# Optimization experiments

Hardware: AMD Instinct MI355X
Metric: run time of the kernel (lower is better)

The kernel has to match this reference:

```python
import jax, jax.numpy as jnp
import numpy as np

KH = KW = 3
SH = SW = 1
PH = PW = 1


def _im2col(x, kh, kw, sh, sw, ph, pw):
    # x: [N, C, H, W] -> cols: [N, C*kh*kw, H_out*W_out], ordering (C, kh, kw)
    N, C, H, W = x.shape
    H_out = (H + 2 * ph - kh) // sh + 1
    W_out = (W + 2 * pw - kw) // sw + 1
    x_pad = jnp.pad(x, ((0, 0), (0, 0), (ph, ph), (pw, pw)))
    # fixed small loop over kernel offsets (kh*kw = 9), strided slices
    patches = [x_pad[:, :, i:i + sh * H_out:sh, j:j + sw * W_out:sw]
               for i in range(kh) for j in range(kw)]  # each [N, C, H_out, W_out]
    cols = jnp.stack(patches, axis=2)  # [N, C, kh*kw, H_out, W_out]
    cols = cols.reshape(N, C * kh * kw, H_out * W_out)
    return cols, H_out, W_out


def setup_inputs() -> dict:
    key = jax.random.key(0)
    k1, k2, k3 = jax.random.split(key, 3)
    x = jax.random.normal(k1, (16, 128, 56, 56), dtype=jnp.float32)
    weight = jax.random.normal(k2, (256, 128, 3, 3), dtype=jnp.float32) * 0.05
    fan_in = 128 * 3 * 3
    bound = 1.0 / fan_in ** 0.5
    bias = jax.random.uniform(k3, (256,), dtype=jnp.float32, minval=-bound, maxval=bound)
    return {"x": x, "weight": weight, "bias": bias}


def reference(x, weight, bias):
    # im2col unfold + (analog) matmul conv; noise_cfg=None -> plain matmul
    cols, H_out, W_out = _im2col(x, KH, KW, SH, SW, PH, PW)  # [N, K, L]
    N = cols.shape[0]
    Cout = weight.shape[0]
    Wmat = weight.reshape(Cout, -1)  # [Cout, K], K = C*kh*kw
    # y[n, l, o] = sum_k cols[n, k, l] * Wmat[o, k]  (AnalogMatMulFn without noise)
    y = jnp.einsum('nkl,ok->nol', cols, Wmat)  # [N, Cout, L]
    y = y.reshape(N, Cout, H_out, W_out)
    y = y + bias[None, :, None, None]
    return y
```

## Files before the change

kernel.cpp:

```cpp
#include <hip/hip_runtime.h>
#include <hip/hip_bf16.h>
#include <stdint.h>


typedef __attribute__((ext_vector_type(8))) short short8;
typedef __attribute__((ext_vector_type(4))) float floatx4;

__device__ static inline void gload_lds16(const void* g, void* l) {
  typedef const __attribute__((address_space(1))) unsigned int* gp_t;
  typedef __attribute__((address_space(3))) unsigned int* lp_t;
  __builtin_amdgcn_global_load_lds((gp_t)(uintptr_t)g, (lp_t)(uint32_t)(uintptr_t)l,
                                   16, 0, 0);
}

__global__ __launch_bounds__(256)
void pre_kernel(const float* __restrict__ x, const float* __restrict__ wsrc,
                __hip_bfloat16* __restrict__ xp, __hip_bfloat16* __restrict__ wt) {
  const int b = blockIdx.x;
  if (b < 16 * 58) {
    const int n = b / 58, hp = b % 58;
    __hip_bfloat16* dst = xp + (size_t)(n * 58 + hp) * 58 * 128;
    if (hp == 0 || hp == 57) {
      const uint4 z = {0, 0, 0, 0};
      uint4* p = (uint4*)dst;
      for (int i = threadIdx.x; i < 928; i += 256) p[i] = z;
      return;
    }
    const int h = hp - 1;
    __shared__ float tile[128][57];
    const float* src = x + (size_t)n * (128 * 3136) + h * 56;
    for (int i = threadIdx.x; i < 128 * 14; i += 256) {
      const int c = i / 14, q = i - c * 14;
      const float4 v = ((const float4*)(src + (size_t)c * 3136))[q];
      tile[c][4 * q + 0] = v.x;
      tile[c][4 * q + 1] = v.y;
      tile[c][4 * q + 2] = v.z;
      tile[c][4 * q + 3] = v.w;
    }
    __syncthreads();
    if (threadIdx.x < 32) {
      const uint4 z = {0, 0, 0, 0};
      const int col = (threadIdx.x >> 4) * 57;
      ((uint4*)(dst + (size_t)col * 128))[threadIdx.x & 15] = z;
    }
    __hip_bfloat16* di = dst + 128;
    for (int i = threadIdx.x; i < 56 * 16; i += 256) {
      const int w = i >> 4, c8 = (i & 15) * 8;
      union { uint4 u; __hip_bfloat16 hh[8]; } pk;
#pragma unroll
      for (int j = 0; j < 8; ++j) pk.hh[j] = __float2bfloat16(tile[c8 + j][w]);
      *(uint4*)(di + (size_t)w * 128 + c8) = pk.u;
    }
  } else {
    const int base = (b - 928) * 256 + threadIdx.x;
    for (int t = base; t < 256 * 9 * 128; t += 36 * 256) {
      const int c = t & 127;
      const int kq = (t >> 7) % 9;
      const int cout = t / (9 * 128);
      wt[t] = __float2bfloat16(wsrc[(size_t)(cout * 128 + c) * 9 + kq]);
    }
  }
}

__global__ __launch_bounds__(256)
void conv_gemm_kernel(const __hip_bfloat16* __restrict__ xp,
                      const __hip_bfloat16* __restrict__ wt,
                      const float* __restrict__ bias,
                      float* __restrict__ out) {
  __shared__ __align__(16) __hip_bfloat16 As[128 * 64];
  __shared__ __align__(16) __hip_bfloat16 Bs[128 * 64];

  const int tid = threadIdx.x;
  const int lane = tid & 63;
  const int wave = tid >> 6;
  const int wm = wave >> 1, wn = wave & 1;

  const int id = blockIdx.x;
  const int xcd = id & 7;
  const int r = id >> 3;
  const int mt_ = r / 49;
  const int nt_ = xcd * 49 + (r - mt_ * 49);
  const int m0 = mt_ * 128;
  const int n0 = nt_ * 128;

  const char* wtb = (const char*)wt;
  const char* xpb = (const char*)xp;
  const char* gA[4];
  const char* gB[4];
  char* lA[4];
  char* lB[4];
#pragma unroll
  for (int i = 0; i < 4; ++i) {
    const int f = (i * 256 + tid) * 16;
    const int row = f >> 7;
    const int sub = (f >> 4) & 7;
    const int cb = (sub ^ (row & 7)) << 4;
    gA[i] = wtb + (size_t)(m0 + row) * 2304 + cb;
    const int pix = n0 + row;
    const int nimg = pix / 3136;
    const int rem = pix - nimg * 3136;
    const int hh = rem / 56;
    const int ww = rem - hh * 56;
    gB[i] = xpb + (size_t)((nimg * 58 + hh) * 58 + ww) * 256 + cb;
    lA[i] = (char*)As + i * 4096 + wave * 1024;
    lB[i] = (char*)Bs + i * 4096 + wave * 1024;
  }

  const int quad = lane >> 4;
  const int x7 = lane & 7;
  const int arow = (wm * 64 + (lane & 15)) * 128;
  const int brow = (wn * 64 + (lane & 15)) * 128;
  int cko[2];
  cko[0] = ((0 + quad) ^ x7) << 4;
  cko[1] = ((4 + quad) ^ x7) << 4;

  floatx4 acc[4][4];
#pragma unroll
  for (int a = 0; a < 4; ++a)
#pragma unroll
    for (int c = 0; c < 4; ++c) acc[a][c] = (floatx4)0.f;

#pragma unroll 1
  for (int kq = 0; kq < 9; ++kq) {
    const int kh = kq / 3;
    const int kw_ = kq - kh * 3;
    const int btap = (kh * 58 + kw_) * 256;
#pragma unroll 1
    for (int ch = 0; ch < 2; ++ch) {
      const int aofs = kq * 256 + ch * 128;
      const int bofs = btap + ch * 128;
      __syncthreads();
#pragma unroll
      for (int i = 0; i < 4; ++i) {
        gload_lds16(gA[i] + aofs, lA[i]);
        gload_lds16(gB[i] + bofs, lB[i]);
      }
      __syncthreads();
#pragma unroll
      for (int ks = 0; ks < 2; ++ks) {
        short8 af[4], bf[4];
#pragma unroll
        for (int mt = 0; mt < 4; ++mt)
          af[mt] = *(const short8*)((const char*)As + arow + mt * (16 * 128) + cko[ks]);
#pragma unroll
        for (int nt = 0; nt < 4; ++nt)
          bf[nt] = *(const short8*)((const char*)Bs + brow + nt * (16 * 128) + cko[ks]);
#pragma unroll
        for (int mt = 0; mt < 4; ++mt)
#pragma unroll
          for (int nt = 0; nt < 4; ++nt)
            acc[mt][nt] = __builtin_amdgcn_mfma_f32_16x16x32_bf16(
                af[mt], bf[nt], acc[mt][nt], 0, 0, 0);
      }
    }
  }

  const int col = lane & 15;
  const int rb = (lane >> 4) * 4;
#pragma unroll
  for (int nt = 0; nt < 4; ++nt) {
    const int pix = n0 + wn * 64 + nt * 16 + col;
    const int nimg = pix / 3136;
    const int rem = pix - nimg * 3136;
    float* op = out + (size_t)nimg * (256 * 3136) + rem;
#pragma unroll
    for (int mt = 0; mt < 4; ++mt) {
      const int mb = m0 + wm * 64 + mt * 16 + rb;
#pragma unroll
      for (int rr = 0; rr < 4; ++rr) {
        op[(size_t)(mb + rr) * 3136] = acc[mt][nt][rr] + bias[mb + rr];
      }
    }
  }
}

__global__ __launch_bounds__(256)
void direct_conv_kernel(const float* __restrict__ x, const float* __restrict__ wgt,
                        const float* __restrict__ bias, float* __restrict__ out) {
  const long t = (long)blockIdx.x * 256 + threadIdx.x;
  if (t >= 16L * 256 * 3136) return;
  const int w = t % 56;
  const int h = (t / 56) % 56;
  const int o = (t / 3136) % 256;
  const int n = t / (256L * 3136);
  float s = bias[o];
  for (int c = 0; c < 128; ++c)
    for (int kh = 0; kh < 3; ++kh) {
      const int hh = h + kh - 1;
      if (hh < 0 || hh >= 56) continue;
      for (int kw = 0; kw < 3; ++kw) {
        const int ww = w + kw - 1;
        if (ww < 0 || ww >= 56) continue;
        s += x[((size_t)(n * 128 + c) * 56 + hh) * 56 + ww] *
             wgt[((size_t)(o * 128 + c) * 3 + kh) * 3 + kw];
      }
    }
  out[t] = s;
}

extern "C" void kernel_launch(void* const* d_in, const int* in_sizes, int n_in,
                              void* d_out, int out_size, void* d_ws, size_t ws_size,
                              hipStream_t stream) {
  const float* x = (const float*)d_in[0];
  const float* w = (const float*)d_in[1];
  const float* b = (const float*)d_in[2];
  float* out = (float*)d_out;

  const size_t xp_bytes = (size_t)16 * 58 * 58 * 128 * 2;
  const size_t wt_bytes = (size_t)256 * 9 * 128 * 2;

  if (ws_size >= xp_bytes + wt_bytes) {
    __hip_bfloat16* xp = (__hip_bfloat16*)d_ws;
    __hip_bfloat16* wt = (__hip_bfloat16*)((char*)d_ws + xp_bytes);
    hipLaunchKernelGGL(pre_kernel, dim3(16 * 58 + 36), dim3(256), 0, stream,
                       x, w, xp, wt);
    hipLaunchKernelGGL(conv_gemm_kernel, dim3(784), dim3(256), 0, stream,
                       xp, wt, b, out);
  } else {
    const long total = 16L * 256 * 3136;
    hipLaunchKernelGGL(direct_conv_kernel, dim3((unsigned)((total + 255) / 256)),
                       dim3(256), 0, stream, x, w, b, out);
  }
}
```

Baseline: 138.2 us.

## Stage an input halo tile in LDS once and double-buffer weight tiles

The output-pixel tile shrinks to 64 and the grid doubles. Each block now loads one contiguous span of 192 padded input pixels into LDS before the main loop. All nine filter taps read their B fragments from that span by row offset, so the input is no longer reloaded per tap. Weight tiles are double-buffered so each step's prefetch overlaps compute, which removes one barrier per step. The cost is about 80KB of LDS per block, lower occupancy, and less MFMA reuse per A fragment.

```diff
diff --git a/kernel.cpp b/kernel.cpp
--- a/kernel.cpp
+++ b/kernel.cpp
@@ -67,8 +67,7 @@
                       const __hip_bfloat16* __restrict__ wt,
                       const float* __restrict__ bias,
                       float* __restrict__ out) {
-  __shared__ __align__(16) __hip_bfloat16 As[128 * 64];
-  __shared__ __align__(16) __hip_bfloat16 Bs[128 * 64];
+  __shared__ __align__(16) char smem[49152 + 2 * 16384];
 
   const int tid = threadIdx.x;
   const int lane = tid & 63;
@@ -78,88 +77,104 @@
   const int id = blockIdx.x;
   const int xcd = id & 7;
   const int r = id >> 3;
-  const int mt_ = r / 49;
-  const int nt_ = xcd * 49 + (r - mt_ * 49);
+  const int mt_ = r / 98;
+  const int nt_ = xcd * 98 + (r - mt_ * 98);
   const int m0 = mt_ * 128;
-  const int n0 = nt_ * 128;
+  const int n0 = nt_ * 64;
+
+  const int nimg0 = n0 / 3136;
+  const int rem0 = n0 - nimg0 * 3136;
+  const int hh0 = rem0 / 56;
+  const int ww0 = rem0 - hh0 * 56;
+  const int P0 = (nimg0 * 58 + hh0) * 58 + ww0;
+  const char* pbase = (const char*)xp + (size_t)P0 * 256;
 
   const char* wtb = (const char*)wt;
-  const char* xpb = (const char*)xp;
   const char* gA[4];
-  const char* gB[4];
-  char* lA[4];
-  char* lB[4];
 #pragma unroll
   for (int i = 0; i < 4; ++i) {
     const int f = (i * 256 + tid) * 16;
-    const int row = f >> 7;
+    const int rowA = f >> 7;
     const int sub = (f >> 4) & 7;
-    const int cb = (sub ^ (row & 7)) << 4;
-    gA[i] = wtb + (size_t)(m0 + row) * 2304 + cb;
-    const int pix = n0 + row;
-    const int nimg = pix / 3136;
-    const int rem = pix - nimg * 3136;
-    const int hh = rem / 56;
-    const int ww = rem - hh * 56;
-    gB[i] = xpb + (size_t)((nimg * 58 + hh) * 58 + ww) * 256 + cb;
-    lA[i] = (char*)As + i * 4096 + wave * 1024;
-    lB[i] = (char*)Bs + i * 4096 + wave * 1024;
-  }
-
+    gA[i] = wtb + (size_t)(m0 + rowA) * 2304 + ((sub ^ (rowA & 7)) << 4);
+  }
+#pragma unroll
+  for (int i = 0; i < 12; ++i) {
+    const int j = i * 256 + tid;
+    const int row = j >> 4;
+    const int slot = j & 15;
+    gload_lds16(pbase + row * 256 + ((slot ^ (row & 7)) << 4),
+                smem + i * 4096 + wave * 1024);
+  }
+#pragma unroll
+  for (int i = 0; i < 4; ++i)
+    gload_lds16(gA[i], smem + 49152 + i * 4096 + wave * 1024);
+
+  const int col = lane & 15;
   const int quad = lane >> 4;
   const int x7 = lane & 7;
-  const int arow = (wm * 64 + (lane & 15)) * 128;
-  const int brow = (wn * 64 + (lane & 15)) * 128;
+  const int arow = (wm * 64 + col) * 128;
   int cko[2];
   cko[0] = ((0 + quad) ^ x7) << 4;
   cko[1] = ((4 + quad) ^ x7) << 4;
-
-  floatx4 acc[4][4];
+  int rbase[2];
+#pragma unroll
+  for (int nt = 0; nt < 2; ++nt) {
+    const int pix = n0 + wn * 32 + nt * 16 + col;
+    const int ni = pix / 3136;
+    const int re = pix - ni * 3136;
+    const int ph = re / 56;
+    const int pw = re - ph * 56;
+    rbase[nt] = (ni * 58 + ph) * 58 + pw - P0;
+  }
+
+  floatx4 acc[4][2];
 #pragma unroll
   for (int a = 0; a < 4; ++a)
 #pragma unroll
-    for (int c = 0; c < 4; ++c) acc[a][c] = (floatx4)0.f;
+    for (int c = 0; c < 2; ++c) acc[a][c] = (floatx4)0.f;
 
 #pragma unroll 1
-  for (int kq = 0; kq < 9; ++kq) {
+  for (int s = 0; s < 18; ++s) {
+    __syncthreads();
+    if (s < 17) {
+      const int s1 = s + 1;
+      const int aofs = (s1 >> 1) * 256 + (s1 & 1) * 128;
+      char* ad = smem + 49152 + ((s1 & 1) << 14) + wave * 1024;
+#pragma unroll
+      for (int i = 0; i < 4; ++i)
+        gload_lds16(gA[i] + aofs, ad + i * 4096);
+    }
+    const int kq = s >> 1, ch = s & 1;
     const int kh = kq / 3;
-    const int kw_ = kq - kh * 3;
-    const int btap = (kh * 58 + kw_) * 256;
-#pragma unroll 1
-    for (int ch = 0; ch < 2; ++ch) {
-      const int aofs = kq * 256 + ch * 128;
-      const int bofs = btap + ch * 128;
-      __syncthreads();
-#pragma unroll
-      for (int i = 0; i < 4; ++i) {
-        gload_lds16(gA[i] + aofs, lA[i]);
-        gload_lds16(gB[i] + bofs, lB[i]);
+    const int tofs = kh * 58 + (kq - kh * 3);
+    const char* ab = smem + 49152 + ((s & 1) << 14);
+#pragma unroll
+    for (int ks = 0; ks < 2; ++ks) {
+      short8 af[4], bf[2];
+#pragma unroll
+      for (int mt = 0; mt < 4; ++mt)
+        af[mt] = *(const short8*)(ab + arow + mt * 2048 + cko[ks]);
+      const int cB = ch * 8 + ks * 4 + quad;
+#pragma unroll
+      for (int nt = 0; nt < 2; ++nt) {
+        const int rowB = rbase[nt] + tofs;
+        const int pos = cB ^ (rowB & 7);
+        bf[nt] = *(const short8*)(smem + rowB * 256 + (pos << 4));
       }
-      __syncthreads();
-#pragma unroll
-      for (int ks = 0; ks < 2; ++ks) {
-        short8 af[4], bf[4];
-#pragma unroll
-        for (int mt = 0; mt < 4; ++mt)
-          af[mt] = *(const short8*)((const char*)As + arow + mt * (16 * 128) + cko[ks]);
-#pragma unroll
-        for (int nt = 0; nt < 4; ++nt)
-          bf[nt] = *(const short8*)((const char*)Bs + brow + nt * (16 * 128) + cko[ks]);
-#pragma unroll
-        for (int mt = 0; mt < 4; ++mt)
-#pragma unroll
-          for (int nt = 0; nt < 4; ++nt)
-            acc[mt][nt] = __builtin_amdgcn_mfma_f32_16x16x32_bf16(
-                af[mt], bf[nt], acc[mt][nt], 0, 0, 0);
-      }
-    }
-  }
-
-  const int col = lane & 15;
-  const int rb = (lane >> 4) * 4;
-#pragma unroll
-  for (int nt = 0; nt < 4; ++nt) {
-    const int pix = n0 + wn * 64 + nt * 16 + col;
+#pragma unroll
+      for (int mt = 0; mt < 4; ++mt)
+#pragma unroll
+        for (int nt = 0; nt < 2; ++nt)
+          acc[mt][nt] = __builtin_amdgcn_mfma_f32_16x16x32_bf16(
+              af[mt], bf[nt], acc[mt][nt], 0, 0, 0);
+    }
+  }
+
+  const int rb = quad * 4;
+#pragma unroll
+  for (int nt = 0; nt < 2; ++nt) {
+    const int pix = n0 + wn * 32 + nt * 16 + col;
     const int nimg = pix / 3136;
     const int rem = pix - nimg * 3136;
     float* op = out + (size_t)nimg * (256 * 3136) + rem;
@@ -214,7 +229,7 @@
     __hip_bfloat16* wt = (__hip_bfloat16*)((char*)d_ws + xp_bytes);
     hipLaunchKernelGGL(pre_kernel, dim3(16 * 58 + 36), dim3(256), 0, stream,
                        x, w, xp, wt);
-    hipLaunchKernelGGL(conv_gemm_kernel, dim3(784), dim3(256), 0, stream,
+    hipLaunchKernelGGL(conv_gemm_kernel, dim3(1568), dim3(256), 0, stream,
                        xp, wt, b, out);
   } else {
     const long total = 16L * 256 * 3136;
```

After: 132.2 us. 4.4% less time.
